# Kernel tuning notes

Hardware: AMD Instinct MI355X
Metric: run time of the kernel (lower is better)

Reference implementation:

```python
import jax, jax.numpy as jnp
import numpy as np

RANK = 16
LN_EPS = 1e-5


def _layer_norm(x, eps=LN_EPS):
    mu = jnp.mean(x, axis=-1, keepdims=True)
    var = jnp.var(x, axis=-1, keepdims=True)
    return (x - mu) / jnp.sqrt(var + eps)


def setup_inputs() -> dict:
    key = jax.random.key(0)
    ks = jax.random.split(key, 8)
    B, S, D, M, R = 32, 4096, 160, 16, RANK
    query = jax.random.normal(ks[0], (B, S, D), dtype=jnp.float32)
    interface = jax.random.normal(ks[1], (B, S, D), dtype=jnp.float32)
    memory = jax.random.normal(ks[2], (B, M, D), dtype=jnp.float32)
    sd = 1.0 / np.sqrt(D)
    sr = 1.0 / np.sqrt(R)
    # torch nn.Linear weights: [out_features, in_features]
    W_read_key = jax.random.uniform(ks[3], (R, D), minval=-sd, maxval=sd, dtype=jnp.float32)
    W_read_value = jax.random.uniform(ks[4], (D, R), minval=-sr, maxval=sr, dtype=jnp.float32)
    W_write_key = jax.random.uniform(ks[5], (R, D), minval=-sd, maxval=sd, dtype=jnp.float32)
    W_write_erase = jax.random.uniform(ks[6], (D, R), minval=-sr, maxval=sr, dtype=jnp.float32)
    W_write_add = jax.random.uniform(ks[7], (D, R), minval=-sr, maxval=sr, dtype=jnp.float32)
    return {
        "query": query,
        "interface": interface,
        "memory": memory,
        "W_read_key": W_read_key,
        "W_read_value": W_read_value,
        "W_write_key": W_write_key,
        "W_write_erase": W_write_erase,
        "W_write_add": W_write_add,
    }


def reference(query, interface, memory, W_read_key, W_read_value,
              W_write_key, W_write_erase, W_write_add):
    R = RANK
    # ---- read ----
    q_proj = jnp.einsum('bsd,rd->bsr', query, W_read_key)          # [B,S,R]
    mem_proj = memory[..., :R]                                      # [B,M,R]
    scores = jnp.einsum('bsr,bmr->bsm', q_proj, mem_proj) / jnp.sqrt(jnp.float32(R))
    attn = jax.nn.softmax(scores, axis=-1)                          # [B,S,M]
    content = jnp.einsum('bsm,bmd->bsd', attn, memory)              # [B,S,D]
    read_out = jnp.einsum('bsr,dr->bsd', content[..., :R], W_read_value)
    # ---- write ----
    i_mean = jnp.mean(interface, axis=1)                            # [B,D]
    i_proj = jnp.einsum('bd,rd->br', i_mean, W_write_key)           # [B,R]
    erase = jax.nn.sigmoid(jnp.einsum('br,dr->bd', i_proj, W_write_erase))[:, None, :]
    add = jnp.einsum('br,dr->bd', i_proj, W_write_add)[:, None, :]
    new_memory = _layer_norm(memory * (1.0 - erase) + add)          # [B,M,D]
    return read_out, new_memory
```

## Files before the change

kernel.cpp:

```cpp
#include <hip/hip_runtime.h>
#include <hip/hip_bf16.h>
#include <math.h>

#define NB 32
#define NS 4096
#define ND 160
#define ND4 40
#define NM 16
#define NR 16
#define TPB 64
#define NCB (NS / TPB)

typedef float  f32x4  __attribute__((ext_vector_type(4)));
typedef short  bf16x8 __attribute__((ext_vector_type(8)));
typedef unsigned int u32x4 __attribute__((ext_vector_type(4)));

__device__ __forceinline__ unsigned bfpair(float lo, float hi) {
    union { float f; unsigned u; } a, c;
    a.f = lo; c.f = hi;
    unsigned ua = (a.u + 0x7FFFu + ((a.u >> 16) & 1u)) >> 16;
    unsigned uc = (c.u + 0x7FFFu + ((c.u >> 16) & 1u)) >> 16;
    return (uc << 16) | (ua & 0xFFFFu);
}

__device__ __forceinline__ bf16x8 asfrag(u32x4 u) {
    union { u32x4 u; bf16x8 h; } x; x.u = u; return x.h;
}

__device__ __forceinline__ bf16x8 mkfrag(unsigned w0, unsigned w1,
                                         unsigned w2, unsigned w3) {
    union { u32x4 u; bf16x8 h; } x;
    x.u = (u32x4){w0, w1, w2, w3};
    return x.h;
}

__global__ __launch_bounds__(256) void ulm_fold_kv(
    const float* __restrict__ memory,
    const float* __restrict__ Wrk,
    const float* __restrict__ Wrv,
    u32x4* __restrict__ kvfrag)
{
    __shared__ __align__(16) float sKV[2 * NM * ND];
    __shared__ float sM16[NM * NR];
    const int b = blockIdx.x;
    const int t = threadIdx.x;

    sM16[t] = memory[((size_t)b * NM + (t >> 4)) * ND + (t & 15)];
    __syncthreads();

    if (t < ND) {
        float wk[NR], wv[NR];
#pragma unroll
        for (int r = 0; r < NR; ++r) wk[r] = Wrk[r * ND + t];
        const float4* wrv4 = reinterpret_cast<const float4*>(Wrv + t * NR);
#pragma unroll
        for (int j = 0; j < 4; ++j) {
            float4 v = wrv4[j];
            wv[j * 4 + 0] = v.x; wv[j * 4 + 1] = v.y;
            wv[j * 4 + 2] = v.z; wv[j * 4 + 3] = v.w;
        }
#pragma unroll
        for (int m = 0; m < NM; ++m) {
            float aK = 0.f, aV = 0.f;
#pragma unroll
            for (int r = 0; r < NR; ++r) {
                float mv = sM16[m * NR + r];
                aK += mv * wk[r];
                aV += mv * wv[r];
            }
            sKV[m * ND + t]           = aK * 0.25f;
            sKV[NM * ND + m * ND + t] = aV;
        }
    }
    __syncthreads();

    u32x4* kb4 = kvfrag + (size_t)b * 640;
    for (int i = t; i < 320; i += 256) {
        int kb = i >> 6, l = i & 63, lr = l & 15, lg = l >> 4;
        const float* s = &sKV[lr * ND + kb * 32 + lg * 8];
        kb4[i] = (u32x4){bfpair(s[0], s[1]), bfpair(s[2], s[3]),
                         bfpair(s[4], s[5]), bfpair(s[6], s[7])};
    }
    for (int i = t; i < 320; i += 256) {
        int d = i >> 5, l = i & 31, lr = l & 15, lg = l >> 4;
        const float* s = &sKV[NM * ND + (lg * 8) * ND + d * 16 + lr];
        kb4[320 + i] = (u32x4){bfpair(s[0 * ND], s[1 * ND]),
                               bfpair(s[2 * ND], s[3 * ND]),
                               bfpair(s[4 * ND], s[5 * ND]),
                               bfpair(s[6 * ND], s[7 * ND])};
    }
}

__global__ __launch_bounds__(256) void ulm_read_kernel(
    const float* __restrict__ query,
    const float* __restrict__ iface,
    const u32x4* __restrict__ kvfrag,
    float* __restrict__ read_out,
    float* __restrict__ ipart)
{
    __shared__ unsigned sP[4][16 * 10];
    __shared__ float4 sIred[4 * ND4];

    const int t = threadIdx.x;
    const int chunk = blockIdx.x;
    const int b = blockIdx.y;
    const int s0 = chunk * TPB;
    const int w  = t >> 6;
    const int l  = t & 63;
    const int lr = l & 15;
    const int lg = l >> 4;

    const size_t base = (size_t)b * NS * ND;
    const int tok = s0 + w * 16 + lr;

    const float4* q4 = reinterpret_cast<const float4*>(query + base);
    float4 qr[10];
#pragma unroll
    for (int kb = 0; kb < 5; ++kb) {
        qr[2*kb]   = q4[(size_t)tok * ND4 + lg * 2 + kb * 8];
        qr[2*kb+1] = q4[(size_t)tok * ND4 + lg * 2 + kb * 8 + 1];
    }

    const u32x4* kvb = kvfrag + (size_t)b * 640;
    u32x4 kfu[5];
#pragma unroll
    for (int kb = 0; kb < 5; ++kb) kfu[kb] = kvb[kb * 64 + l];
    u32x4 vfu[10];
#pragma unroll
    for (int d = 0; d < 10; ++d)
        vfu[d] = (lg < 2) ? kvb[320 + d * 32 + (l & 31)]
                          : (u32x4){0u, 0u, 0u, 0u};

    f32x4 D = {0.f, 0.f, 0.f, 0.f};
#pragma unroll
    for (int kb = 0; kb < 5; ++kb) {
        bf16x8 qf = mkfrag(bfpair(qr[2*kb].x,   qr[2*kb].y),
                           bfpair(qr[2*kb].z,   qr[2*kb].w),
                           bfpair(qr[2*kb+1].x, qr[2*kb+1].y),
                           bfpair(qr[2*kb+1].z, qr[2*kb+1].w));
        D = __builtin_amdgcn_mfma_f32_16x16x32_bf16(asfrag(kfu[kb]), qf, D, 0, 0, 0);
    }

    float mx = fmaxf(fmaxf(D[0], D[1]), fmaxf(D[2], D[3]));
    mx = fmaxf(mx, __shfl_xor(mx, 16));
    mx = fmaxf(mx, __shfl_xor(mx, 32));
    float e0 = __expf(D[0] - mx), e1 = __expf(D[1] - mx);
    float e2 = __expf(D[2] - mx), e3 = __expf(D[3] - mx);
    float sm = e0 + e1 + e2 + e3;
    sm += __shfl_xor(sm, 16);
    sm += __shfl_xor(sm, 32);
    float inv = 1.f / sm;
    e0 *= inv; e1 *= inv; e2 *= inv; e3 *= inv;

    unsigned* pl = &sP[w][0];
    pl[lr * 10 + lg * 2 + 0] = bfpair(e0, e1);
    pl[lr * 10 + lg * 2 + 1] = bfpair(e2, e3);
    asm volatile("s_waitcnt lgkmcnt(0)" ::: "memory");
    int pb = (lg < 2) ? (lr * 10 + lg * 4) : 0;
    bf16x8 pf = mkfrag(pl[pb], pl[pb + 1], pl[pb + 2], pl[pb + 3]);

    const float4* i4 = reinterpret_cast<const float4*>(iface + base);
    const int l8 = l & 7, g8 = l >> 3;
    const int itok = s0 + w * 16 + g8 * 2;
    float4 iv[10];
#pragma unroll
    for (int j = 0; j < 2; ++j)
#pragma unroll
        for (int k = 0; k < 5; ++k)
            iv[j * 5 + k] = i4[(size_t)(itok + j) * ND4 + l8 + 8 * k];

    float4* out4 = reinterpret_cast<float4*>(read_out + base);
#pragma unroll
    for (int d = 0; d < 10; ++d) {
        f32x4 D2 = {0.f, 0.f, 0.f, 0.f};
        D2 = __builtin_amdgcn_mfma_f32_16x16x32_bf16(asfrag(vfu[d]), pf, D2, 0, 0, 0);
        out4[(size_t)tok * ND4 + d * 4 + lg] = make_float4(D2[0], D2[1], D2[2], D2[3]);
    }

#pragma unroll
    for (int k = 0; k < 5; ++k) {
        float x = iv[k].x + iv[5 + k].x, y = iv[k].y + iv[5 + k].y;
        float z = iv[k].z + iv[5 + k].z, u = iv[k].w + iv[5 + k].w;
#pragma unroll
        for (int off = 8; off <= 32; off <<= 1) {
            x += __shfl_xor(x, off); y += __shfl_xor(y, off);
            z += __shfl_xor(z, off); u += __shfl_xor(u, off);
        }
        if (l < 8) sIred[w * ND4 + k * 8 + l8] = make_float4(x, y, z, u);
    }
    __syncthreads();
    if (t < ND4) {
        float4 a0 = sIred[t], a1 = sIred[ND4 + t];
        float4 a2 = sIred[2 * ND4 + t], a3 = sIred[3 * ND4 + t];
        float4 tot = make_float4(a0.x + a1.x + a2.x + a3.x,
                                 a0.y + a1.y + a2.y + a3.y,
                                 a0.z + a1.z + a2.z + a3.z,
                                 a0.w + a1.w + a2.w + a3.w);
        reinterpret_cast<float4*>(ipart + ((size_t)(b * NCB + chunk)) * ND)[t] = tot;
    }
}

__global__ __launch_bounds__(256) void ulm_write_kernel(
    const float* __restrict__ memory,
    const float* __restrict__ Wwk,
    const float* __restrict__ Wwe,
    const float* __restrict__ Wwa,
    const float* __restrict__ ipart,
    float* __restrict__ new_mem)
{
    __shared__ float sIm[ND];
    __shared__ float sIp[NR];
    __shared__ float sOmE[ND];
    __shared__ float sAdd[ND];

    const int b = blockIdx.x;
    const int t = threadIdx.x;

    if (t < ND) {
        float acc = 0.f;
#pragma unroll 8
        for (int c = 0; c < NCB; ++c)
            acc += ipart[((size_t)(b * NCB + c)) * ND + t];
        sIm[t] = acc * (1.0f / NS);
    }
    __syncthreads();

    if (t < NR) {
        float acc = 0.f;
        for (int d = 0; d < ND; ++d) acc += sIm[d] * Wwk[t * ND + d];
        sIp[t] = acc;
    }
    __syncthreads();

    if (t < ND) {
        float e = 0.f, a = 0.f;
#pragma unroll
        for (int r = 0; r < NR; ++r) {
            float ip = sIp[r];
            e += ip * Wwe[t * NR + r];
            a += ip * Wwa[t * NR + r];
        }
        sOmE[t] = 1.0f - 1.0f / (1.0f + __expf(-e));
        sAdd[t] = a;
    }
    __syncthreads();

    const int wave = t >> 6, lane = t & 63;
    for (int m = wave; m < NM; m += 4) {
        const float* mrow = memory + ((size_t)b * NM + m) * ND;
        float v0 = mrow[lane] * sOmE[lane] + sAdd[lane];
        float v1 = mrow[lane + 64] * sOmE[lane + 64] + sAdd[lane + 64];
        float v2 = 0.f;
        const bool has2 = lane < 32;
        if (has2) v2 = mrow[lane + 128] * sOmE[lane + 128] + sAdd[lane + 128];
        float s  = v0 + v1 + v2;
        float sq = v0 * v0 + v1 * v1 + v2 * v2;
#pragma unroll
        for (int off = 32; off; off >>= 1) {
            s  += __shfl_xor(s, off);
            sq += __shfl_xor(sq, off);
        }
        float mu   = s * (1.0f / ND);
        float var  = sq * (1.0f / ND) - mu * mu;
        float rstd = rsqrtf(var + 1e-5f);
        float* orow = new_mem + ((size_t)b * NM + m) * ND;
        orow[lane]      = (v0 - mu) * rstd;
        orow[lane + 64] = (v1 - mu) * rstd;
        if (has2) orow[lane + 128] = (v2 - mu) * rstd;
    }
}

extern "C" void kernel_launch(void* const* d_in, const int* in_sizes, int n_in,
                              void* d_out, int out_size, void* d_ws, size_t ws_size,
                              hipStream_t stream) {
    const float* query  = (const float*)d_in[0];
    const float* iface  = (const float*)d_in[1];
    const float* memory = (const float*)d_in[2];
    const float* Wrk    = (const float*)d_in[3];
    const float* Wrv    = (const float*)d_in[4];
    const float* Wwk    = (const float*)d_in[5];
    const float* Wwe    = (const float*)d_in[6];
    const float* Wwa    = (const float*)d_in[7];

    float* read_out = (float*)d_out;
    float* new_mem  = (float*)d_out + (size_t)NB * NS * ND;
    float* ipart    = (float*)d_ws;
    u32x4* kvfrag   = (u32x4*)((float*)d_ws + (size_t)NB * NCB * ND);

    ulm_fold_kv<<<NB, 256, 0, stream>>>(memory, Wrk, Wrv, kvfrag);
    dim3 grid1(NCB, NB);
    ulm_read_kernel<<<grid1, 256, 0, stream>>>(query, iface, kvfrag,
                                               read_out, ipart);
    ulm_write_kernel<<<NB, 256, 0, stream>>>(memory, Wwk, Wwe, Wwa, ipart, new_mem);
}
```

Before: 59.06 us.

## Fuse write kernel into read kernel via last-block atomic counter per batch

Removes the separate write kernel launch. Each read block publishes its partial interface sum, then bumps a per-batch atomic counter, and the last block to finish for that batch does the mean, projection, erase/add and layer norm. The fold kernel resets the counters. The interface loads are also hoisted ahead of the softmax so they overlap with the MFMA work. This trades a launch and its dependency gap for a threadfence, an atomic, extra shared memory and more register pressure in the read kernel.

```diff
diff --git a/kernel.cpp b/kernel.cpp
--- a/kernel.cpp
+++ b/kernel.cpp
@@ -38,12 +38,15 @@
     const float* __restrict__ memory,
     const float* __restrict__ Wrk,
     const float* __restrict__ Wrv,
-    u32x4* __restrict__ kvfrag)
+    u32x4* __restrict__ kvfrag,
+    unsigned* __restrict__ counters)
 {
     __shared__ __align__(16) float sKV[2 * NM * ND];
     __shared__ float sM16[NM * NR];
     const int b = blockIdx.x;
     const int t = threadIdx.x;
+
+    if (t == 0) counters[b] = 0u;
 
     sM16[t] = memory[((size_t)b * NM + (t >> 4)) * ND + (t & 15)];
     __syncthreads();
@@ -94,12 +97,23 @@
 __global__ __launch_bounds__(256) void ulm_read_kernel(
     const float* __restrict__ query,
     const float* __restrict__ iface,
+    const float* __restrict__ memory,
     const u32x4* __restrict__ kvfrag,
+    const float* __restrict__ Wwk,
+    const float* __restrict__ Wwe,
+    const float* __restrict__ Wwa,
     float* __restrict__ read_out,
-    float* __restrict__ ipart)
+    float* __restrict__ new_mem,
+    float* __restrict__ ipart,
+    unsigned* __restrict__ counters)
 {
     __shared__ unsigned sP[4][16 * 10];
     __shared__ float4 sIred[4 * ND4];
+    __shared__ int sLast;
+    __shared__ float sIm[ND];
+    __shared__ float sIp[NR];
+    __shared__ float sOmE[ND];
+    __shared__ float sAdd[ND];
 
     const int t = threadIdx.x;
     const int chunk = blockIdx.x;
@@ -140,6 +154,16 @@
                            bfpair(qr[2*kb+1].z, qr[2*kb+1].w));
         D = __builtin_amdgcn_mfma_f32_16x16x32_bf16(asfrag(kfu[kb]), qf, D, 0, 0, 0);
     }
+
+    const float4* i4 = reinterpret_cast<const float4*>(iface + base);
+    const int l8 = l & 7, g8 = l >> 3;
+    const int itok = s0 + w * 16 + g8 * 2;
+    float4 iv[10];
+#pragma unroll
+    for (int j = 0; j < 2; ++j)
+#pragma unroll
+        for (int k = 0; k < 5; ++k)
+            iv[j * 5 + k] = i4[(size_t)(itok + j) * ND4 + l8 + 8 * k];
 
     float mx = fmaxf(fmaxf(D[0], D[1]), fmaxf(D[2], D[3]));
     mx = fmaxf(mx, __shfl_xor(mx, 16));
@@ -159,16 +183,6 @@
     int pb = (lg < 2) ? (lr * 10 + lg * 4) : 0;
     bf16x8 pf = mkfrag(pl[pb], pl[pb + 1], pl[pb + 2], pl[pb + 3]);
 
-    const float4* i4 = reinterpret_cast<const float4*>(iface + base);
-    const int l8 = l & 7, g8 = l >> 3;
-    const int itok = s0 + w * 16 + g8 * 2;
-    float4 iv[10];
-#pragma unroll
-    for (int j = 0; j < 2; ++j)
-#pragma unroll
-        for (int k = 0; k < 5; ++k)
-            iv[j * 5 + k] = i4[(size_t)(itok + j) * ND4 + l8 + 8 * k];
-
     float4* out4 = reinterpret_cast<float4*>(read_out + base);
 #pragma unroll
     for (int d = 0; d < 10; ++d) {
@@ -197,24 +211,17 @@
                                  a0.z + a1.z + a2.z + a3.z,
                                  a0.w + a1.w + a2.w + a3.w);
         reinterpret_cast<float4*>(ipart + ((size_t)(b * NCB + chunk)) * ND)[t] = tot;
-    }
-}
-
-__global__ __launch_bounds__(256) void ulm_write_kernel(
-    const float* __restrict__ memory,
-    const float* __restrict__ Wwk,
-    const float* __restrict__ Wwe,
-    const float* __restrict__ Wwa,
-    const float* __restrict__ ipart,
-    float* __restrict__ new_mem)
-{
-    __shared__ float sIm[ND];
-    __shared__ float sIp[NR];
-    __shared__ float sOmE[ND];
-    __shared__ float sAdd[ND];
-
-    const int b = blockIdx.x;
-    const int t = threadIdx.x;
+        __threadfence();
+    }
+    __syncthreads();
+    if (t == 0) {
+        unsigned old = atomicAdd(&counters[b], 1u);
+        sLast = (old == NCB - 1);
+    }
+    __syncthreads();
+    if (!sLast) return;
+
+    __threadfence();
 
     if (t < ND) {
         float acc = 0.f;
@@ -245,8 +252,8 @@
     }
     __syncthreads();
 
-    const int wave = t >> 6, lane = t & 63;
-    for (int m = wave; m < NM; m += 4) {
+    const int lane = l;
+    for (int m = w; m < NM; m += 4) {
         const float* mrow = memory + ((size_t)b * NM + m) * ND;
         float v0 = mrow[lane] * sOmE[lane] + sAdd[lane];
         float v1 = mrow[lane + 64] * sOmE[lane + 64] + sAdd[lane + 64];
@@ -284,12 +291,14 @@
 
     float* read_out = (float*)d_out;
     float* new_mem  = (float*)d_out + (size_t)NB * NS * ND;
-    float* ipart    = (float*)d_ws;
-    u32x4* kvfrag   = (u32x4*)((float*)d_ws + (size_t)NB * NCB * ND);
-
-    ulm_fold_kv<<<NB, 256, 0, stream>>>(memory, Wrk, Wrv, kvfrag);
+
+    float*    ipart    = (float*)d_ws;
+    u32x4*    kvfrag   = (u32x4*)(ipart + (size_t)NB * NCB * ND);
+    unsigned* counters = (unsigned*)(kvfrag + (size_t)NB * 640);
+
+    ulm_fold_kv<<<NB, 256, 0, stream>>>(memory, Wrk, Wrv, kvfrag, counters);
     dim3 grid1(NCB, NB);
-    ulm_read_kernel<<<grid1, 256, 0, stream>>>(query, iface, kvfrag,
-                                               read_out, ipart);
-    ulm_write_kernel<<<NB, 256, 0, stream>>>(memory, Wwk, Wwe, Wwa, ipart, new_mem);
-}
+    ulm_read_kernel<<<grid1, 256, 0, stream>>>(query, iface, memory, kvfrag,
+                                               Wwk, Wwe, Wwa,
+                                               read_out, new_mem, ipart, counters);
+}
```

Result: slower. 167.4 us (+183.4%).

## Fuse K/V folding into read kernel via chained MFMA projections

Applied to the files above, without the earlier changes.

Removes the separate fold kernel that precomputed memory·W_read_key and memory·W_read_value fragments. The read kernel now projects queries with W_read_key, scores against memory, applies softmax, gathers memory columns and projects with W_read_value, all as chained small MFMAs with LDS transposes between stages. This saves one kernel launch and the workspace round trip. In exchange each block repeats the weight loads, bf16 conversions and extra MFMA stages, and rounds intermediates to bf16 more often. It also switches the bf16 conversion to the HIP intrinsic.

```diff
diff --git a/kernel.cpp b/kernel.cpp
--- a/kernel.cpp
+++ b/kernel.cpp
@@ -15,90 +15,30 @@
 typedef short  bf16x8 __attribute__((ext_vector_type(8)));
 typedef unsigned int u32x4 __attribute__((ext_vector_type(4)));
 
+__device__ __forceinline__ unsigned short f2bf(float f) {
+    union { __hip_bfloat16 b; unsigned short s; } x;
+    x.b = __float2bfloat16(f);
+    return x.s;
+}
 __device__ __forceinline__ unsigned bfpair(float lo, float hi) {
-    union { float f; unsigned u; } a, c;
-    a.f = lo; c.f = hi;
-    unsigned ua = (a.u + 0x7FFFu + ((a.u >> 16) & 1u)) >> 16;
-    unsigned uc = (c.u + 0x7FFFu + ((c.u >> 16) & 1u)) >> 16;
-    return (uc << 16) | (ua & 0xFFFFu);
-}
-
+    return ((unsigned)f2bf(hi) << 16) | (unsigned)f2bf(lo);
+}
 __device__ __forceinline__ bf16x8 asfrag(u32x4 u) {
     union { u32x4 u; bf16x8 h; } x; x.u = u; return x.h;
 }
 
-__device__ __forceinline__ bf16x8 mkfrag(unsigned w0, unsigned w1,
-                                         unsigned w2, unsigned w3) {
-    union { u32x4 u; bf16x8 h; } x;
-    x.u = (u32x4){w0, w1, w2, w3};
-    return x.h;
-}
-
-__global__ __launch_bounds__(256) void ulm_fold_kv(
+__global__ __launch_bounds__(256) void ulm_read_kernel(
+    const float* __restrict__ query,
+    const float* __restrict__ iface,
     const float* __restrict__ memory,
     const float* __restrict__ Wrk,
     const float* __restrict__ Wrv,
-    u32x4* __restrict__ kvfrag)
-{
-    __shared__ __align__(16) float sKV[2 * NM * ND];
-    __shared__ float sM16[NM * NR];
-    const int b = blockIdx.x;
-    const int t = threadIdx.x;
-
-    sM16[t] = memory[((size_t)b * NM + (t >> 4)) * ND + (t & 15)];
-    __syncthreads();
-
-    if (t < ND) {
-        float wk[NR], wv[NR];
-#pragma unroll
-        for (int r = 0; r < NR; ++r) wk[r] = Wrk[r * ND + t];
-        const float4* wrv4 = reinterpret_cast<const float4*>(Wrv + t * NR);
-#pragma unroll
-        for (int j = 0; j < 4; ++j) {
-            float4 v = wrv4[j];
-            wv[j * 4 + 0] = v.x; wv[j * 4 + 1] = v.y;
-            wv[j * 4 + 2] = v.z; wv[j * 4 + 3] = v.w;
-        }
-#pragma unroll
-        for (int m = 0; m < NM; ++m) {
-            float aK = 0.f, aV = 0.f;
-#pragma unroll
-            for (int r = 0; r < NR; ++r) {
-                float mv = sM16[m * NR + r];
-                aK += mv * wk[r];
-                aV += mv * wv[r];
-            }
-            sKV[m * ND + t]           = aK * 0.25f;
-            sKV[NM * ND + m * ND + t] = aV;
-        }
-    }
-    __syncthreads();
-
-    u32x4* kb4 = kvfrag + (size_t)b * 640;
-    for (int i = t; i < 320; i += 256) {
-        int kb = i >> 6, l = i & 63, lr = l & 15, lg = l >> 4;
-        const float* s = &sKV[lr * ND + kb * 32 + lg * 8];
-        kb4[i] = (u32x4){bfpair(s[0], s[1]), bfpair(s[2], s[3]),
-                         bfpair(s[4], s[5]), bfpair(s[6], s[7])};
-    }
-    for (int i = t; i < 320; i += 256) {
-        int d = i >> 5, l = i & 31, lr = l & 15, lg = l >> 4;
-        const float* s = &sKV[NM * ND + (lg * 8) * ND + d * 16 + lr];
-        kb4[320 + i] = (u32x4){bfpair(s[0 * ND], s[1 * ND]),
-                               bfpair(s[2 * ND], s[3 * ND]),
-                               bfpair(s[4 * ND], s[5 * ND]),
-                               bfpair(s[6 * ND], s[7 * ND])};
-    }
-}
-
-__global__ __launch_bounds__(256) void ulm_read_kernel(
-    const float* __restrict__ query,
-    const float* __restrict__ iface,
-    const u32x4* __restrict__ kvfrag,
     float* __restrict__ read_out,
     float* __restrict__ ipart)
 {
-    __shared__ unsigned sP[4][16 * 10];
+    __shared__ unsigned sG[4][160];
+    __shared__ unsigned sPm[4][160];
+    __shared__ unsigned sH[4][160];
     __shared__ float4 sIred[4 * ND4];
 
     const int t = threadIdx.x;
@@ -109,6 +49,7 @@
     const int l  = t & 63;
     const int lr = l & 15;
     const int lg = l >> 4;
+    const bool lo2 = (lg < 2);
 
     const size_t base = (size_t)b * NS * ND;
     const int tok = s0 + w * 16 + lr;
@@ -121,60 +62,111 @@
         qr[2*kb+1] = q4[(size_t)tok * ND4 + lg * 2 + kb * 8 + 1];
     }
 
-    const u32x4* kvb = kvfrag + (size_t)b * 640;
-    u32x4 kfu[5];
-#pragma unroll
-    for (int kb = 0; kb < 5; ++kb) kfu[kb] = kvb[kb * 64 + l];
-    u32x4 vfu[10];
-#pragma unroll
-    for (int d = 0; d < 10; ++d)
-        vfu[d] = (lg < 2) ? kvb[320 + d * 32 + (l & 31)]
-                          : (u32x4){0u, 0u, 0u, 0u};
-
-    f32x4 D = {0.f, 0.f, 0.f, 0.f};
+    const float4* wk4 = reinterpret_cast<const float4*>(Wrk);
+    u32x4 wf[5];
 #pragma unroll
     for (int kb = 0; kb < 5; ++kb) {
-        bf16x8 qf = mkfrag(bfpair(qr[2*kb].x,   qr[2*kb].y),
+        float4 a = wk4[lr * ND4 + kb * 8 + lg * 2];
+        float4 c = wk4[lr * ND4 + kb * 8 + lg * 2 + 1];
+        wf[kb] = (u32x4){bfpair(a.x, a.y), bfpair(a.z, a.w),
+                         bfpair(c.x, c.y), bfpair(c.z, c.w)};
+    }
+
+    f32x4 G = {0.f, 0.f, 0.f, 0.f};
+#pragma unroll
+    for (int kb = 0; kb < 5; ++kb) {
+        u32x4 qf = (u32x4){bfpair(qr[2*kb].x,   qr[2*kb].y),
                            bfpair(qr[2*kb].z,   qr[2*kb].w),
                            bfpair(qr[2*kb+1].x, qr[2*kb+1].y),
-                           bfpair(qr[2*kb+1].z, qr[2*kb+1].w));
-        D = __builtin_amdgcn_mfma_f32_16x16x32_bf16(asfrag(kfu[kb]), qf, D, 0, 0, 0);
-    }
-
-    float mx = fmaxf(fmaxf(D[0], D[1]), fmaxf(D[2], D[3]));
+                           bfpair(qr[2*kb+1].z, qr[2*kb+1].w)};
+        G = __builtin_amdgcn_mfma_f32_16x16x32_bf16(asfrag(wf[kb]), asfrag(qf), G, 0, 0, 0);
+    }
+
+    unsigned* gl = &sG[w][0];
+    gl[lr * 10 + lg * 2 + 0] = bfpair(G[0], G[1]);
+    gl[lr * 10 + lg * 2 + 1] = bfpair(G[2], G[3]);
+    asm volatile("s_waitcnt lgkmcnt(0)" ::: "memory");
+    int gb = lo2 ? (lr * 10 + lg * 4) : 0;
+    u32x4 gf = (u32x4){gl[gb], gl[gb + 1], gl[gb + 2], gl[gb + 3]};
+
+    u32x4 mf = (u32x4){0u, 0u, 0u, 0u};
+    if (lo2) {
+        const float4* m4 = reinterpret_cast<const float4*>(
+            memory + ((size_t)b * NM + lr) * ND + lg * 8);
+        float4 a = m4[0], c = m4[1];
+        mf = (u32x4){bfpair(0.25f * a.x, 0.25f * a.y),
+                     bfpair(0.25f * a.z, 0.25f * a.w),
+                     bfpair(0.25f * c.x, 0.25f * c.y),
+                     bfpair(0.25f * c.z, 0.25f * c.w)};
+    }
+    f32x4 S = {0.f, 0.f, 0.f, 0.f};
+    S = __builtin_amdgcn_mfma_f32_16x16x32_bf16(asfrag(mf), asfrag(gf), S, 0, 0, 0);
+
+    const float4* i4 = reinterpret_cast<const float4*>(iface + base);
+    const int l8 = l & 7, g8 = l >> 3;
+    const int itok = s0 + w * 16 + g8 * 2;
+    float4 iv[10];
+#pragma unroll
+    for (int j = 0; j < 2; ++j)
+#pragma unroll
+        for (int k = 0; k < 5; ++k)
+            iv[j * 5 + k] = i4[(size_t)(itok + j) * ND4 + l8 + 8 * k];
+
+    float mx = fmaxf(fmaxf(S[0], S[1]), fmaxf(S[2], S[3]));
     mx = fmaxf(mx, __shfl_xor(mx, 16));
     mx = fmaxf(mx, __shfl_xor(mx, 32));
-    float e0 = __expf(D[0] - mx), e1 = __expf(D[1] - mx);
-    float e2 = __expf(D[2] - mx), e3 = __expf(D[3] - mx);
+    float e0 = __expf(S[0] - mx), e1 = __expf(S[1] - mx);
+    float e2 = __expf(S[2] - mx), e3 = __expf(S[3] - mx);
     float sm = e0 + e1 + e2 + e3;
     sm += __shfl_xor(sm, 16);
     sm += __shfl_xor(sm, 32);
     float inv = 1.f / sm;
     e0 *= inv; e1 *= inv; e2 *= inv; e3 *= inv;
 
-    unsigned* pl = &sP[w][0];
+    unsigned* pl = &sPm[w][0];
     pl[lr * 10 + lg * 2 + 0] = bfpair(e0, e1);
     pl[lr * 10 + lg * 2 + 1] = bfpair(e2, e3);
     asm volatile("s_waitcnt lgkmcnt(0)" ::: "memory");
-    int pb = (lg < 2) ? (lr * 10 + lg * 4) : 0;
-    bf16x8 pf = mkfrag(pl[pb], pl[pb + 1], pl[pb + 2], pl[pb + 3]);
-
-    const float4* i4 = reinterpret_cast<const float4*>(iface + base);
-    const int l8 = l & 7, g8 = l >> 3;
-    const int itok = s0 + w * 16 + g8 * 2;
-    float4 iv[10];
-#pragma unroll
-    for (int j = 0; j < 2; ++j)
-#pragma unroll
-        for (int k = 0; k < 5; ++k)
-            iv[j * 5 + k] = i4[(size_t)(itok + j) * ND4 + l8 + 8 * k];
-
+    int pb = lo2 ? (lr * 10 + lg * 4) : 0;
+    u32x4 pf = (u32x4){pl[pb], pl[pb + 1], pl[pb + 2], pl[pb + 3]};
+
+    u32x4 mtf = (u32x4){0u, 0u, 0u, 0u};
+    if (lo2) {
+        float f0 = memory[((size_t)b * NM + lg * 8 + 0) * ND + lr];
+        float f1 = memory[((size_t)b * NM + lg * 8 + 1) * ND + lr];
+        float f2 = memory[((size_t)b * NM + lg * 8 + 2) * ND + lr];
+        float f3 = memory[((size_t)b * NM + lg * 8 + 3) * ND + lr];
+        float f4 = memory[((size_t)b * NM + lg * 8 + 4) * ND + lr];
+        float f5 = memory[((size_t)b * NM + lg * 8 + 5) * ND + lr];
+        float f6 = memory[((size_t)b * NM + lg * 8 + 6) * ND + lr];
+        float f7 = memory[((size_t)b * NM + lg * 8 + 7) * ND + lr];
+        mtf = (u32x4){bfpair(f0, f1), bfpair(f2, f3),
+                      bfpair(f4, f5), bfpair(f6, f7)};
+    }
+    f32x4 H = {0.f, 0.f, 0.f, 0.f};
+    H = __builtin_amdgcn_mfma_f32_16x16x32_bf16(asfrag(mtf), asfrag(pf), H, 0, 0, 0);
+
+    unsigned* hl = &sH[w][0];
+    hl[lr * 10 + lg * 2 + 0] = bfpair(H[0], H[1]);
+    hl[lr * 10 + lg * 2 + 1] = bfpair(H[2], H[3]);
+    asm volatile("s_waitcnt lgkmcnt(0)" ::: "memory");
+    int hb = lo2 ? (lr * 10 + lg * 4) : 0;
+    u32x4 hf = (u32x4){hl[hb], hl[hb + 1], hl[hb + 2], hl[hb + 3]};
+
+    const float4* wv4 = reinterpret_cast<const float4*>(Wrv);
     float4* out4 = reinterpret_cast<float4*>(read_out + base);
 #pragma unroll
-    for (int d = 0; d < 10; ++d) {
-        f32x4 D2 = {0.f, 0.f, 0.f, 0.f};
-        D2 = __builtin_amdgcn_mfma_f32_16x16x32_bf16(asfrag(vfu[d]), pf, D2, 0, 0, 0);
-        out4[(size_t)tok * ND4 + d * 4 + lg] = make_float4(D2[0], D2[1], D2[2], D2[3]);
+    for (int db = 0; db < 10; ++db) {
+        u32x4 vf = (u32x4){0u, 0u, 0u, 0u};
+        if (lo2) {
+            float4 a = wv4[(db * 16 + lr) * 4 + lg * 2];
+            float4 c = wv4[(db * 16 + lr) * 4 + lg * 2 + 1];
+            vf = (u32x4){bfpair(a.x, a.y), bfpair(a.z, a.w),
+                         bfpair(c.x, c.y), bfpair(c.z, c.w)};
+        }
+        f32x4 C = {0.f, 0.f, 0.f, 0.f};
+        C = __builtin_amdgcn_mfma_f32_16x16x32_bf16(asfrag(vf), asfrag(hf), C, 0, 0, 0);
+        out4[(size_t)tok * ND4 + db * 4 + lg] = make_float4(C[0], C[1], C[2], C[3]);
     }
 
 #pragma unroll
@@ -285,11 +277,9 @@
     float* read_out = (float*)d_out;
     float* new_mem  = (float*)d_out + (size_t)NB * NS * ND;
     float* ipart    = (float*)d_ws;
-    u32x4* kvfrag   = (u32x4*)((float*)d_ws + (size_t)NB * NCB * ND);
-
-    ulm_fold_kv<<<NB, 256, 0, stream>>>(memory, Wrk, Wrv, kvfrag);
+
     dim3 grid1(NCB, NB);
-    ulm_read_kernel<<<grid1, 256, 0, stream>>>(query, iface, kvfrag,
+    ulm_read_kernel<<<grid1, 256, 0, stream>>>(query, iface, memory, Wrk, Wrv,
                                                read_out, ipart);
     ulm_write_kernel<<<NB, 256, 0, stream>>>(memory, Wwk, Wwe, Wwa, ipart, new_mem);
 }
```

Measured after the change: 58.19 us. Within noise of the previous version (-1.5%).
